# Performance work log

Measured on AMD Instinct MI355X. Metric: run time of the kernel, lower is better.

The kernel has to match this reference:

```python
import jax, jax.numpy as jnp
import numpy as np

B, N1, N2, D, H = 32, 512, 256, 256, 8
HD = D // H  # head dim = 32


def setup_inputs() -> dict:
    key = jax.random.key(0)
    ks = jax.random.split(key, 12)
    s = 0.05
    return {
        "x1": jax.random.normal(ks[0], (B, N1, D), jnp.float32),
        "x2": jax.random.normal(ks[1], (B, N2, D), jnp.float32),
        "r_w1": jax.random.normal(ks[2], (D, 2 * D), jnp.float32) * s,
        "r_b1": jnp.zeros((D,), jnp.float32),
        "ln_g": jnp.ones((D,), jnp.float32),
        "ln_b": jnp.zeros((D,), jnp.float32),
        "r_w2": jax.random.normal(ks[3], (4, D), jnp.float32) * s,
        "r_b2": jnp.zeros((4,), jnp.float32),
        "lf_w": jax.random.normal(ks[4], (D, D), jnp.float32) * s,
        "lf_b": jnp.zeros((D,), jnp.float32),
        "af2_w": jax.random.normal(ks[5], (D, D), jnp.float32) * s,
        "af2_b": jnp.zeros((D,), jnp.float32),
        "af3_w": jax.random.normal(ks[6], (N1, D), jnp.float32) * s,  # Linear(dim, num_pathway)
        "af3_b": jnp.zeros((N1,), jnp.float32),
        "attn_in_w": jax.random.normal(ks[7], (3 * D, D), jnp.float32) * s,
        "attn_in_b": jnp.zeros((3 * D,), jnp.float32),
        "attn_out_w": jax.random.normal(ks[8], (D, D), jnp.float32) * s,
        "attn_out_b": jnp.zeros((D,), jnp.float32),
    }


def _layernorm(x, g, b, eps=1e-5):
    mu = x.mean(-1, keepdims=True)
    var = ((x - mu) ** 2).mean(-1, keepdims=True)
    return (x - mu) * jax.lax.rsqrt(var + eps) * g + b


def reference(x1, x2, r_w1, r_b1, ln_g, ln_b, r_w2, r_b2,
              lf_w, lf_b, af2_w, af2_b, af3_w, af3_b,
              attn_in_w, attn_in_b, attn_out_w, attn_out_b):
    b, n1, d = x1.shape
    n2 = x2.shape[1]

    # ---- RoutingNetwork: mean-pool both modalities, small MLP, softmax ----
    m = jnp.concatenate([x1.mean(1), x2.mean(1)], axis=-1)        # [b, 2d]
    h = jax.nn.gelu(_layernorm(m @ r_w1.T + r_b1, ln_g, ln_b), approximate=False)
    logits = h @ r_w2.T + r_b2                                     # [b, 4]
    w = jax.nn.softmax(logits, axis=-1)                            # [b, 4]

    z = jnp.concatenate([x1, x2], axis=1)                          # [b, n1+n2, d]

    # ---- Expert 0: LinearFusion (dropout off at eval) ----
    lf = jax.nn.elu(z @ lf_w.T + lf_b)
    g0, i0 = lf[:, :n1, :], lf[:, n1:, :]

    # ---- Expert 1: AddFusion, n1 >= n2 branch (n2 == dim required) ----
    a1 = jax.nn.elu(x1 @ af2_w.T + af2_b)                          # [b, n1, d]
    a2 = jax.nn.elu(jnp.einsum('bnd,pn->bdp', x2, af3_w) + af3_b)  # [b, d, n1]
    a2 = a2.transpose(0, 2, 1)                                     # [b, n1, d]
    x_out = a1 + a2
    g1, i1 = x_out, x_out[:, :n2, :]

    # ---- Expert 2: AttentionFusion (MHA, 8 heads, self-attn over concat) ----
    qkv = z @ attn_in_w.T + attn_in_b                              # [b, S, 3d]
    q, k, v = jnp.split(qkv, 3, axis=-1)
    S = n1 + n2
    q = q.reshape(b, S, H, HD)
    k = k.reshape(b, S, H, HD)
    v = v.reshape(b, S, H, HD)
    scores = jnp.einsum('bqhd,bkhd->bhqk', q, k) / np.sqrt(HD)
    attn = jax.nn.softmax(scores, axis=-1)
    o = jnp.einsum('bhqk,bkhd->bqhd', attn, v).reshape(b, S, d)
    o = o @ attn_out_w.T + attn_out_b
    g2, i2 = o[:, :n1, :], o[:, n1:, :]

    # ---- Expert 3: IdentityFusion ----
    g3, i3 = x1, x2

    # ---- Soft-routing weighted combine ----
    gene_all = jnp.stack([g0, g1, g2, g3], axis=1)                 # [b, 4, n1, d]
    img_all = jnp.stack([i0, i1, i2, i3], axis=1)                  # [b, 4, n2, d]
    we = w[:, :, None, None]
    gene = (gene_all * we).sum(axis=1)
    img = (img_all * we).sum(axis=1)
    return gene, img
```

## Files before the change

kernel.cpp:

```cpp
#include <hip/hip_runtime.h>
#include <hip/hip_bf16.h>
#include <math.h>

#define B_ 32
#define N1_ 512
#define N2_ 256
#define D_ 256
#define S_ 768
#define IMG_OFF 4194304
#define SCALE_ 0.17677669529663689f

typedef __attribute__((ext_vector_type(8))) short bf16x8;
typedef __attribute__((ext_vector_type(4))) float f32x4;
#define MFMA16(a, b, c) __builtin_amdgcn_mfma_f32_16x16x32_bf16(a, b, c, 0, 0, 0)

__device__ __forceinline__ ushort f2b(float f) {
  __hip_bfloat16 h = __float2bfloat16(f);
  return __builtin_bit_cast(ushort, h);
}
__device__ __forceinline__ float eluf(float v) { return v > 0.f ? v : expm1f(v); }

__global__ __launch_bounds__(256) void k_cvt(const float* __restrict__ src,
                                             ushort* __restrict__ zb,
                                             int shift, int boff) {
  int j = blockIdx.x*256 + threadIdx.x;
  int b = j >> shift;
  int rj = j & ((1 << shift) - 1);
  const float4* s = (const float4*)src + (size_t)j*2;
  float4 v0 = s[0], v1 = s[1];
  uint4 pk;
  pk.x = (uint)f2b(v0.x) | ((uint)f2b(v0.y) << 16);
  pk.y = (uint)f2b(v0.z) | ((uint)f2b(v0.w) << 16);
  pk.z = (uint)f2b(v1.x) | ((uint)f2b(v1.y) << 16);
  pk.w = (uint)f2b(v1.z) | ((uint)f2b(v1.w) << 16);
  *(uint4*)(zb + (size_t)b*196608 + boff + (size_t)rj*8) = pk;
}

__global__ __launch_bounds__(256) void k_wcvt(const float* __restrict__ lf_w,
                                              const float* __restrict__ af2_w,
                                              const float* __restrict__ af3_w,
                                              const float* __restrict__ attn_in_w,
                                              const float* __restrict__ attn_out_w,
                                              ushort* __restrict__ wb) {
  int g = blockIdx.x*256 + threadIdx.x;
  int e0 = g*4;
  const float* src; int loc; float sc = 1.f;
  if (e0 < 65536)       { src = lf_w;       loc = e0; }
  else if (e0 < 131072) { src = af2_w;      loc = e0 - 65536; }
  else if (e0 < 262144) { src = af3_w;      loc = e0 - 131072; }
  else if (e0 < 458752) { src = attn_in_w;  loc = e0 - 262144; if (loc < 65536) sc = SCALE_; }
  else                  { src = attn_out_w; loc = e0 - 458752; }
  float4 v = *(const float4*)(src + loc);
  *(ushort4*)(wb + e0) = make_ushort4(f2b(v.x*sc), f2b(v.y*sc), f2b(v.z*sc), f2b(v.w*sc));
}

__global__ __launch_bounds__(256) void k_mean(const float* __restrict__ x1,
                                              const float* __restrict__ x2,
                                              float* __restrict__ mp) {
  int b = blockIdx.x >> 3;
  int s = blockIdx.x & 7;
  int d = threadIdx.x;
  float s1 = 0.f;
  const float* p1 = x1 + ((size_t)(b*N1_ + s*64))*D_ + d;
  for (int n = 0; n < 64; ++n) s1 += p1[(size_t)n*D_];
  float s2 = 0.f;
  const float* p2 = x2 + ((size_t)(b*N2_ + s*32))*D_ + d;
  for (int n = 0; n < 32; ++n) s2 += p2[(size_t)n*D_];
  mp[(size_t)(b*8+s)*512 + d]       = s1 * (1.0f/512.0f);
  mp[(size_t)(b*8+s)*512 + 256 + d] = s2 * (1.0f/256.0f);
}

__global__ __launch_bounds__(256) void k_head(const float* __restrict__ mp, const float* __restrict__ r_w1,
                       const float* __restrict__ r_b1, const float* __restrict__ ln_g,
                       const float* __restrict__ ln_b, const float* __restrict__ r_w2,
                       const float* __restrict__ r_b2, float* __restrict__ wout) {
  int b = blockIdx.x;
  int j = threadIdx.x;
  __shared__ float ms[512];
  __shared__ float red[256];
  float a0 = 0.f, a1 = 0.f;
  for (int s = 0; s < 8; ++s) {
    a0 += mp[(size_t)(b*8+s)*512 + j];
    a1 += mp[(size_t)(b*8+s)*512 + 256 + j];
  }
  ms[j] = a0; ms[j+256] = a1;
  __syncthreads();
  float acc = r_b1[j];
  const float* wrow = r_w1 + (size_t)j*512;
  for (int k = 0; k < 512; ++k) acc += ms[k]*wrow[k];
  red[j] = acc; __syncthreads();
  for (int off=128; off>0; off>>=1){ if (j<off) red[j]+=red[j+off]; __syncthreads(); }
  float mu = red[0] * (1.f/256.f); __syncthreads();
  float cd = acc - mu;
  red[j] = cd*cd; __syncthreads();
  for (int off=128; off>0; off>>=1){ if (j<off) red[j]+=red[j+off]; __syncthreads(); }
  float var = red[0]*(1.f/256.f); __syncthreads();
  float xn = cd * rsqrtf(var + 1e-5f) * ln_g[j] + ln_b[j];
  float h = 0.5f*xn*(1.f+erff(xn*0.70710678118654752f));
  float lg[4];
  for (int e=0;e<4;++e){
    red[j] = h * r_w2[e*256 + j]; __syncthreads();
    for (int off=128; off>0; off>>=1){ if (j<off) red[j]+=red[j+off]; __syncthreads(); }
    lg[e] = red[0] + r_b2[e]; __syncthreads();
  }
  if (j==0){
    float mx = fmaxf(fmaxf(lg[0],lg[1]),fmaxf(lg[2],lg[3]));
    float e0=expf(lg[0]-mx),e1=expf(lg[1]-mx),e2=expf(lg[2]-mx),e3=expf(lg[3]-mx);
    float s=e0+e1+e2+e3;
    wout[b*4+0]=e0/s; wout[b*4+1]=e1/s; wout[b*4+2]=e2/s; wout[b*4+3]=e3/s;
  }
}

__global__ __launch_bounds__(256) void k_lf(const ushort* __restrict__ zb, const ushort* __restrict__ wb,
                     const float* __restrict__ x1, const float* __restrict__ x2,
                     const float* __restrict__ lf_b,
                     const float* __restrict__ wgt, float* __restrict__ out) {
  int dt = blockIdx.x, nt = blockIdx.y, b = blockIdx.z;
  int tid = threadIdx.x;
  int lane = tid & 63, wid = tid >> 6;
  int wm = wid >> 1, wn = wid & 1;
  int l15 = lane & 15, quad = lane >> 4;
  __shared__ __align__(16) ushort As[64][72];
  __shared__ __align__(16) ushort Ws[64][72];
  f32x4 acc[2][2] = {};
  int n0 = nt*64, d0 = dt*64;
  int sr = tid >> 2, scg = (tid & 3) * 16;
  const ushort* arow = zb + (size_t)b*196608 + (size_t)(n0+sr)*256;
  const ushort* wrow = wb + (size_t)(d0+sr)*256;
  for (int k0 = 0; k0 < 256; k0 += 64) {
    *(uint4*)&As[sr][scg]   = *(const uint4*)(arow + k0 + scg);
    *(uint4*)&As[sr][scg+8] = *(const uint4*)(arow + k0 + scg + 8);
    *(uint4*)&Ws[sr][scg]   = *(const uint4*)(wrow + k0 + scg);
    *(uint4*)&Ws[sr][scg+8] = *(const uint4*)(wrow + k0 + scg + 8);
    __syncthreads();
    #pragma unroll
    for (int kc = 0; kc < 2; ++kc) {
      bf16x8 a0f = *(bf16x8*)&As[wm*32 + l15][kc*32 + quad*8];
      bf16x8 a1f = *(bf16x8*)&As[wm*32 + 16 + l15][kc*32 + quad*8];
      bf16x8 b0f = *(bf16x8*)&Ws[wn*32 + l15][kc*32 + quad*8];
      bf16x8 b1f = *(bf16x8*)&Ws[wn*32 + 16 + l15][kc*32 + quad*8];
      acc[0][0] = MFMA16(a0f, b0f, acc[0][0]);
      acc[0][1] = MFMA16(a0f, b1f, acc[0][1]);
      acc[1][0] = MFMA16(a1f, b0f, acc[1][0]);
      acc[1][1] = MFMA16(a1f, b1f, acc[1][1]);
    }
    __syncthreads();
  }
  float w0 = wgt[b*4+0], w3 = wgt[b*4+3];
  #pragma unroll
  for (int im = 0; im < 2; ++im) {
    #pragma unroll
    for (int reg = 0; reg < 4; ++reg) {
      int n = n0 + wm*32 + im*16 + quad*4 + reg;
      const float* zr = (n<N1_)? x1 + ((size_t)(b*N1_+n))*D_ : x2 + ((size_t)(b*N2_+(n-N1_)))*D_;
      float* orw = (n<N1_)? out + ((size_t)(b*N1_+n))*D_
                          : out + (size_t)IMG_OFF + ((size_t)(b*N2_+(n-N1_)))*D_;
      #pragma unroll
      for (int in = 0; in < 2; ++in) {
        int d = d0 + wn*32 + in*16 + l15;
        float v = acc[im][in][reg] + lf_b[d];
        orw[d] = w0*eluf(v) + w3*zr[d];
      }
    }
  }
}

__global__ __launch_bounds__(256) void k_xout(const ushort* __restrict__ zb, const ushort* __restrict__ wb,
                       const float* __restrict__ af2_b, const float* __restrict__ af3_b,
                       const float* __restrict__ wgt, float* __restrict__ out) {
  int dt = blockIdx.x, nt = blockIdx.y, b = blockIdx.z;
  int tid = threadIdx.x;
  int lane = tid & 63, wid = tid >> 6;
  int wm = wid >> 1, wn = wid & 1;
  int l15 = lane & 15, quad = lane >> 4;
  __shared__ __align__(16) ushort As1[64][72];
  __shared__ __align__(16) ushort Ws1[64][72];
  __shared__ __align__(16) ushort As2[64][72];
  __shared__ __align__(16) ushort Ws2[64][72];
  f32x4 acc1[2][2] = {}, acc2[2][2] = {};
  int n0 = nt*64, d0 = dt*64;
  int sr = tid >> 2, scg = (tid & 3) * 16;
  const ushort* a1row = zb + (size_t)b*196608 + (size_t)(n0+sr)*256;
  const ushort* w1row = wb + 65536 + (size_t)(d0+sr)*256;
  const ushort* a2row = wb + 131072 + (size_t)(n0+sr)*256;
  for (int k0 = 0; k0 < 256; k0 += 64) {
    *(uint4*)&As1[sr][scg]   = *(const uint4*)(a1row + k0 + scg);
    *(uint4*)&As1[sr][scg+8] = *(const uint4*)(a1row + k0 + scg + 8);
    *(uint4*)&Ws1[sr][scg]   = *(const uint4*)(w1row + k0 + scg);
    *(uint4*)&Ws1[sr][scg+8] = *(const uint4*)(w1row + k0 + scg + 8);
    *(uint4*)&As2[sr][scg]   = *(const uint4*)(a2row + k0 + scg);
    *(uint4*)&As2[sr][scg+8] = *(const uint4*)(a2row + k0 + scg + 8);
    {
      const ushort* x2r = zb + (size_t)b*196608 + 131072 + (size_t)(k0+sr)*256 + d0 + scg;
      uint4 va = *(const uint4*)x2r;
      uint4 vb = *(const uint4*)(x2r + 8);
      const ushort* ea = (const ushort*)&va;
      const ushort* eb = (const ushort*)&vb;
      #pragma unroll
      for (int i = 0; i < 8; ++i) Ws2[scg + i][sr] = ea[i];
      #pragma unroll
      for (int i = 0; i < 8; ++i) Ws2[scg + 8 + i][sr] = eb[i];
    }
    __syncthreads();
    #pragma unroll
    for (int kc = 0; kc < 2; ++kc) {
      bf16x8 a10 = *(bf16x8*)&As1[wm*32 + l15][kc*32 + quad*8];
      bf16x8 a11 = *(bf16x8*)&As1[wm*32 + 16 + l15][kc*32 + quad*8];
      bf16x8 b10 = *(bf16x8*)&Ws1[wn*32 + l15][kc*32 + quad*8];
      bf16x8 b11 = *(bf16x8*)&Ws1[wn*32 + 16 + l15][kc*32 + quad*8];
      acc1[0][0] = MFMA16(a10, b10, acc1[0][0]);
      acc1[0][1] = MFMA16(a10, b11, acc1[0][1]);
      acc1[1][0] = MFMA16(a11, b10, acc1[1][0]);
      acc1[1][1] = MFMA16(a11, b11, acc1[1][1]);
      bf16x8 a20 = *(bf16x8*)&As2[wm*32 + l15][kc*32 + quad*8];
      bf16x8 a21 = *(bf16x8*)&As2[wm*32 + 16 + l15][kc*32 + quad*8];
      bf16x8 b20 = *(bf16x8*)&Ws2[wn*32 + l15][kc*32 + quad*8];
      bf16x8 b21 = *(bf16x8*)&Ws2[wn*32 + 16 + l15][kc*32 + quad*8];
      acc2[0][0] = MFMA16(a20, b20, acc2[0][0]);
      acc2[0][1] = MFMA16(a20, b21, acc2[0][1]);
      acc2[1][0] = MFMA16(a21, b20, acc2[1][0]);
      acc2[1][1] = MFMA16(a21, b21, acc2[1][1]);
    }
    __syncthreads();
  }
  float w1v = wgt[b*4+1];
  #pragma unroll
  for (int im = 0; im < 2; ++im) {
    #pragma unroll
    for (int reg = 0; reg < 4; ++reg) {
      int n = n0 + wm*32 + im*16 + quad*4 + reg;
      float* grow = out + ((size_t)(b*N1_+n))*D_;
      float* irow = (n<N2_)? (out + (size_t)IMG_OFF + ((size_t)(b*N2_+n))*D_) : nullptr;
      float b3 = af3_b[n];
      #pragma unroll
      for (int in = 0; in < 2; ++in) {
        int d = d0 + wn*32 + in*16 + l15;
        float xo = eluf(acc1[im][in][reg] + af2_b[d]) + eluf(acc2[im][in][reg] + b3);
        grow[d] += w1v*xo;
        if (irow) irow[d] += w1v*xo;
      }
    }
  }
}

__global__ __launch_bounds__(256) void k_qkv(const ushort* __restrict__ zb, const ushort* __restrict__ wb,
                      const float* __restrict__ bias,
                      ushort* __restrict__ qws, ushort* __restrict__ kws,
                      ushort* __restrict__ vtws) {
  int ct = blockIdx.x, nt = blockIdx.y, b = blockIdx.z;
  int tid = threadIdx.x;
  int lane = tid & 63, wid = tid >> 6;
  int wm = wid >> 1, wn = wid & 1;
  int l15 = lane & 15, quad = lane >> 4;
  __shared__ __align__(16) ushort As[64][72];
  __shared__ __align__(16) ushort Ws[64][72];
  f32x4 acc[2][2] = {};
  int n0 = nt*64, c0b = ct*64;
  int sr = tid >> 2, scg = (tid & 3) * 16;
  const ushort* arow = zb + (size_t)b*196608 + (size_t)(n0+sr)*256;
  const ushort* wrow = wb + 262144 + (size_t)(c0b+sr)*256;
  for (int k0 = 0; k0 < 256; k0 += 64) {
    *(uint4*)&As[sr][scg]   = *(const uint4*)(arow + k0 + scg);
    *(uint4*)&As[sr][scg+8] = *(const uint4*)(arow + k0 + scg + 8);
    *(uint4*)&Ws[sr][scg]   = *(const uint4*)(wrow + k0 + scg);
    *(uint4*)&Ws[sr][scg+8] = *(const uint4*)(wrow + k0 + scg + 8);
    __syncthreads();
    #pragma unroll
    for (int kc = 0; kc < 2; ++kc) {
      bf16x8 a0f = *(bf16x8*)&As[wm*32 + l15][kc*32 + quad*8];
      bf16x8 a1f = *(bf16x8*)&As[wm*32 + 16 + l15][kc*32 + quad*8];
      bf16x8 b0f = *(bf16x8*)&Ws[wn*32 + l15][kc*32 + quad*8];
      bf16x8 b1f = *(bf16x8*)&Ws[wn*32 + 16 + l15][kc*32 + quad*8];
      acc[0][0] = MFMA16(a0f, b0f, acc[0][0]);
      acc[0][1] = MFMA16(a0f, b1f, acc[0][1]);
      acc[1][0] = MFMA16(a1f, b0f, acc[1][0]);
      acc[1][1] = MFMA16(a1f, b1f, acc[1][1]);
    }
    __syncthreads();
  }
  if (ct < 8) {
    ushort* dst = (ct < 4) ? qws : kws;
    int coff = (ct < 4) ? 0 : 256;
    float bsc = (ct < 4) ? SCALE_ : 1.f;
    #pragma unroll
    for (int im = 0; im < 2; ++im) {
      #pragma unroll
      for (int reg = 0; reg < 4; ++reg) {
        int n = n0 + wm*32 + im*16 + quad*4 + reg;
        #pragma unroll
        for (int in = 0; in < 2; ++in) {
          int c = c0b + wn*32 + in*16 + l15;
          dst[((size_t)(b*S_)+n)*256 + (c - coff)] = f2b(acc[im][in][reg] + bias[c]*bsc);
        }
      }
    }
  } else {
    #pragma unroll
    for (int im = 0; im < 2; ++im) {
      int nb = n0 + wm*32 + im*16 + quad*4;
      #pragma unroll
      for (int in = 0; in < 2; ++in) {
        int c = c0b + wn*32 + in*16 + l15;
        float bs = bias[c];
        int vcol = c - 512;
        int h = vcol >> 5, d = vcol & 31;
        uint2 pk;
        pk.x = (uint)f2b(acc[im][in][0] + bs) | ((uint)f2b(acc[im][in][1] + bs) << 16);
        pk.y = (uint)f2b(acc[im][in][2] + bs) | ((uint)f2b(acc[im][in][3] + bs) << 16);
        *(uint2*)&vtws[(((size_t)(b*8+h))*32 + d)*S_ + nb] = pk;
      }
    }
  }
}

__global__ __launch_bounds__(256) void k_attn(const ushort* __restrict__ qws,
                                              const ushort* __restrict__ kws,
                                              const ushort* __restrict__ vtws,
                                              ushort* __restrict__ obuf) {
  int qt = blockIdx.x, h = blockIdx.y, b = blockIdx.z;
  int tid = threadIdx.x;
  int lane = tid & 63, w = tid >> 6;
  int l15 = lane & 15, quad = lane >> 4;
  __shared__ __align__(16) ushort Ks[64][40];
  __shared__ __align__(16) ushort Vts[32][72];
  __shared__ __align__(16) ushort Ps[4][16][72];

  bf16x8 bq[2];
  #pragma unroll
  for (int u = 0; u < 2; ++u) {
    int qn = qt*128 + w*32 + u*16 + l15;
    bq[u] = *(const bf16x8*)(qws + ((size_t)(b*S_)+qn)*256 + h*32 + quad*8);
  }
  f32x4 ao[2][2] = {};
  float m_run[2] = {-INFINITY, -INFINITY};
  float l_run[2] = {0.f, 0.f};

  int skr = tid >> 2, skc = (tid & 3) * 8;
  int svd = tid >> 3, svn = (tid & 7) * 8;

  for (int kt = 0; kt < 12; ++kt) {
    __syncthreads();
    *(uint4*)&Ks[skr][skc] =
        *(const uint4*)(kws + ((size_t)(b*S_) + kt*64 + skr)*256 + h*32 + skc);
    *(uint4*)&Vts[svd][svn] =
        *(const uint4*)(vtws + (((size_t)(b*8+h))*32 + svd)*S_ + kt*64 + svn);
    __syncthreads();

    bf16x8 ak[4];
    #pragma unroll
    for (int t = 0; t < 4; ++t) ak[t] = *(bf16x8*)&Ks[t*16 + l15][quad*8];
    bf16x8 av[2][2];
    #pragma unroll
    for (int im = 0; im < 2; ++im)
      #pragma unroll
      for (int kc = 0; kc < 2; ++kc)
        av[im][kc] = *(bf16x8*)&Vts[im*16 + l15][kc*32 + quad*8];

    #pragma unroll
    for (int u = 0; u < 2; ++u) {
      f32x4 sf[4];
      #pragma unroll
      for (int t = 0; t < 4; ++t) {
        f32x4 z = {0.f, 0.f, 0.f, 0.f};
        sf[t] = MFMA16(ak[t], bq[u], z);
      }
      float m0 = sf[0][0];
      #pragma unroll
      for (int t = 0; t < 4; ++t)
        #pragma unroll
        for (int r = 0; r < 4; ++r) m0 = fmaxf(m0, sf[t][r]);
      m0 = fmaxf(m0, __shfl_xor(m0, 16, 64));
      m0 = fmaxf(m0, __shfl_xor(m0, 32, 64));
      float mnew = fmaxf(m_run[u], m0);
      float al = __expf(m_run[u] - mnew);
      m_run[u] = mnew;
      float ls = 0.f;
      ushort pu[4][4];
      #pragma unroll
      for (int t = 0; t < 4; ++t)
        #pragma unroll
        for (int r = 0; r < 4; ++r) {
          float p = __expf(sf[t][r] - mnew);
          ls += p;
          pu[t][r] = f2b(p);
        }
      ls += __shfl_xor(ls, 16, 64);
      ls += __shfl_xor(ls, 32, 64);
      l_run[u] = l_run[u]*al + ls;
      #pragma unroll
      for (int t = 0; t < 4; ++t) {
        uint2 pk;
        pk.x = (uint)pu[t][0] | ((uint)pu[t][1] << 16);
        pk.y = (uint)pu[t][2] | ((uint)pu[t][3] << 16);
        *(uint2*)&Ps[w][l15][t*16 + quad*4] = pk;
      }
      #pragma unroll
      for (int e = 0; e < 4; ++e) { ao[u][0][e] *= al; ao[u][1][e] *= al; }
      #pragma unroll
      for (int kc = 0; kc < 2; ++kc) {
        bf16x8 bp = *(bf16x8*)&Ps[w][l15][kc*32 + quad*8];
        ao[u][0] = MFMA16(av[0][kc], bp, ao[u][0]);
        ao[u][1] = MFMA16(av[1][kc], bp, ao[u][1]);
      }
    }
  }
  #pragma unroll
  for (int u = 0; u < 2; ++u) {
    float linv = 1.f / l_run[u];
    int n = qt*128 + w*32 + u*16 + l15;
    ushort* orow = obuf + ((size_t)(b*S_)+n)*256 + h*32;
    #pragma unroll
    for (int im = 0; im < 2; ++im) {
      uint2 pk;
      pk.x = (uint)f2b(ao[u][im][0]*linv) | ((uint)f2b(ao[u][im][1]*linv) << 16);
      pk.y = (uint)f2b(ao[u][im][2]*linv) | ((uint)f2b(ao[u][im][3]*linv) << 16);
      *(uint2*)(orow + im*16 + quad*4) = pk;
    }
  }
}

__global__ __launch_bounds__(256) void k_proj(const ushort* __restrict__ obuf, const ushort* __restrict__ wb,
                       const float* __restrict__ bias, const float* __restrict__ wgt,
                       float* __restrict__ out) {
  int dt = blockIdx.x, nt = blockIdx.y, b = blockIdx.z;
  int tid = threadIdx.x;
  int lane = tid & 63, wid = tid >> 6;
  int wm = wid >> 1, wn = wid & 1;
  int l15 = lane & 15, quad = lane >> 4;
  __shared__ __align__(16) ushort As[64][72];
  __shared__ __align__(16) ushort Ws[64][72];
  f32x4 acc[2][2] = {};
  int n0 = nt*64, d0 = dt*64;
  int sr = tid >> 2, scg = (tid & 3) * 16;
  const ushort* arow = obuf + ((size_t)(b*S_) + n0 + sr)*256;
  const ushort* wrow = wb + 458752 + (size_t)(d0+sr)*256;
  for (int k0 = 0; k0 < 256; k0 += 64) {
    *(uint4*)&As[sr][scg]   = *(const uint4*)(arow + k0 + scg);
    *(uint4*)&As[sr][scg+8] = *(const uint4*)(arow + k0 + scg + 8);
    *(uint4*)&Ws[sr][scg]   = *(const uint4*)(wrow + k0 + scg);
    *(uint4*)&Ws[sr][scg+8] = *(const uint4*)(wrow + k0 + scg + 8);
    __syncthreads();
    #pragma unroll
    for (int kc = 0; kc < 2; ++kc) {
      bf16x8 a0f = *(bf16x8*)&As[wm*32 + l15][kc*32 + quad*8];
      bf16x8 a1f = *(bf16x8*)&As[wm*32 + 16 + l15][kc*32 + quad*8];
      bf16x8 b0f = *(bf16x8*)&Ws[wn*32 + l15][kc*32 + quad*8];
      bf16x8 b1f = *(bf16x8*)&Ws[wn*32 + 16 + l15][kc*32 + quad*8];
      acc[0][0] = MFMA16(a0f, b0f, acc[0][0]);
      acc[0][1] = MFMA16(a0f, b1f, acc[0][1]);
      acc[1][0] = MFMA16(a1f, b0f, acc[1][0]);
      acc[1][1] = MFMA16(a1f, b1f, acc[1][1]);
    }
    __syncthreads();
  }
  float w2v = wgt[b*4+2];
  #pragma unroll
  for (int im = 0; im < 2; ++im) {
    #pragma unroll
    for (int reg = 0; reg < 4; ++reg) {
      int n = n0 + wm*32 + im*16 + quad*4 + reg;
      float* orw = (n<N1_)? out + ((size_t)(b*N1_+n))*D_
                          : out + (size_t)IMG_OFF + ((size_t)(b*N2_+(n-N1_)))*D_;
      #pragma unroll
      for (int in = 0; in < 2; ++in) {
        int d = d0 + wn*32 + in*16 + l15;
        orw[d] += w2v*(acc[im][in][reg] + bias[d]);
      }
    }
  }
}

extern "C" void kernel_launch(void* const* d_in, const int* in_sizes, int n_in,
                              void* d_out, int out_size, void* d_ws, size_t ws_size,
                              hipStream_t stream) {
  const float* x1        = (const float*)d_in[0];
  const float* x2        = (const float*)d_in[1];
  const float* r_w1      = (const float*)d_in[2];
  const float* r_b1      = (const float*)d_in[3];
  const float* ln_g      = (const float*)d_in[4];
  const float* ln_b      = (const float*)d_in[5];
  const float* r_w2      = (const float*)d_in[6];
  const float* r_b2      = (const float*)d_in[7];
  const float* lf_w      = (const float*)d_in[8];
  const float* lf_b      = (const float*)d_in[9];
  const float* af2_w     = (const float*)d_in[10];
  const float* af2_b     = (const float*)d_in[11];
  const float* af3_w     = (const float*)d_in[12];
  const float* af3_b     = (const float*)d_in[13];
  const float* attn_in_w = (const float*)d_in[14];
  const float* attn_in_b = (const float*)d_in[15];
  const float* attn_out_w= (const float*)d_in[16];
  const float* attn_out_b= (const float*)d_in[17];
  float* out = (float*)d_out;

  float* ws_mp = (float*)d_ws;
  float* ws_w  = ws_mp + 131072;
  ushort* ws_qo = (ushort*)(ws_w + 128);
  ushort* ws_k  = ws_qo + (size_t)B_*S_*256;
  ushort* ws_vt = ws_k  + (size_t)B_*S_*256;
  ushort* ws_zb = ws_vt + (size_t)B_*S_*256;
  ushort* ws_wb = ws_zb + (size_t)B_*S_*256;

  k_cvt <<<dim3(2048), 256, 0, stream>>>(x1, ws_zb, 14, 0);
  k_cvt <<<dim3(1024), 256, 0, stream>>>(x2, ws_zb, 13, 131072);
  k_wcvt<<<dim3(512),  256, 0, stream>>>(lf_w, af2_w, af3_w, attn_in_w, attn_out_w, ws_wb);
  k_mean<<<dim3(B_*8), 256, 0, stream>>>(x1, x2, ws_mp);
  k_head<<<dim3(B_),   256, 0, stream>>>(ws_mp, r_w1, r_b1, ln_g, ln_b, r_w2, r_b2, ws_w);
  k_lf  <<<dim3(4,12,B_), 256, 0, stream>>>(ws_zb, ws_wb, x1, x2, lf_b, ws_w, out);
  k_xout<<<dim3(4,8,B_),  256, 0, stream>>>(ws_zb, ws_wb, af2_b, af3_b, ws_w, out);
  k_qkv <<<dim3(12,12,B_),256, 0, stream>>>(ws_zb, ws_wb, attn_in_b, ws_qo, ws_k, ws_vt);
  k_attn<<<dim3(6,8,B_),  256, 0, stream>>>(ws_qo, ws_k, ws_vt, ws_qo);
  k_proj<<<dim3(4,12,B_), 256, 0, stream>>>(ws_qo, attn_out_w ? ws_wb : ws_wb, attn_out_b, ws_w, out);
}
```

Before: 285.7 us.

## Fuse expert GEMMs into one output kernel and drop online softmax max

```diff
diff --git a/kernel.cpp b/kernel.cpp
--- a/kernel.cpp
+++ b/kernel.cpp
@@ -9,6 +9,7 @@
 #define S_ 768
 #define IMG_OFF 4194304
 #define SCALE_ 0.17677669529663689f
+#define QSCALE_ (0.17677669529663689f * 1.4426950408889634f)
 
 typedef __attribute__((ext_vector_type(8))) short bf16x8;
 typedef __attribute__((ext_vector_type(4))) float f32x4;
@@ -20,20 +21,48 @@
 }
 __device__ __forceinline__ float eluf(float v) { return v > 0.f ? v : expm1f(v); }
 
-__global__ __launch_bounds__(256) void k_cvt(const float* __restrict__ src,
-                                             ushort* __restrict__ zb,
-                                             int shift, int boff) {
-  int j = blockIdx.x*256 + threadIdx.x;
-  int b = j >> shift;
-  int rj = j & ((1 << shift) - 1);
-  const float4* s = (const float4*)src + (size_t)j*2;
-  float4 v0 = s[0], v1 = s[1];
-  uint4 pk;
-  pk.x = (uint)f2b(v0.x) | ((uint)f2b(v0.y) << 16);
-  pk.y = (uint)f2b(v0.z) | ((uint)f2b(v0.w) << 16);
-  pk.z = (uint)f2b(v1.x) | ((uint)f2b(v1.y) << 16);
-  pk.w = (uint)f2b(v1.z) | ((uint)f2b(v1.w) << 16);
-  *(uint4*)(zb + (size_t)b*196608 + boff + (size_t)rj*8) = pk;
+__global__ __launch_bounds__(256) void k_prep(const float* __restrict__ x1,
+                                              const float* __restrict__ x2,
+                                              ushort* __restrict__ zb,
+                                              float* __restrict__ mp) {
+  int b = blockIdx.x >> 3, s = blockIdx.x & 7;
+  int t = threadIdx.x;
+  int c = t & 63;
+  int rg = t >> 6;
+  __shared__ float red[4][260];
+  float4 s1 = {0.f, 0.f, 0.f, 0.f};
+  for (int i = 0; i < 16; ++i) {
+    int r = s*64 + rg*16 + i;
+    float4 v = *(const float4*)(x1 + ((size_t)(b*N1_) + r)*D_ + c*4);
+    s1.x += v.x; s1.y += v.y; s1.z += v.z; s1.w += v.w;
+    uint2 pk;
+    pk.x = (uint)f2b(v.x) | ((uint)f2b(v.y) << 16);
+    pk.y = (uint)f2b(v.z) | ((uint)f2b(v.w) << 16);
+    *(uint2*)(zb + (size_t)b*196608 + (size_t)r*256 + c*4) = pk;
+  }
+  red[rg][c*4+0] = s1.x; red[rg][c*4+1] = s1.y; red[rg][c*4+2] = s1.z; red[rg][c*4+3] = s1.w;
+  __syncthreads();
+  {
+    float v = red[0][t] + red[1][t] + red[2][t] + red[3][t];
+    mp[(size_t)(b*8+s)*512 + t] = v * (1.0f/512.0f);
+  }
+  __syncthreads();
+  float4 s2 = {0.f, 0.f, 0.f, 0.f};
+  for (int i = 0; i < 8; ++i) {
+    int r = s*32 + rg*8 + i;
+    float4 v = *(const float4*)(x2 + ((size_t)(b*N2_) + r)*D_ + c*4);
+    s2.x += v.x; s2.y += v.y; s2.z += v.z; s2.w += v.w;
+    uint2 pk;
+    pk.x = (uint)f2b(v.x) | ((uint)f2b(v.y) << 16);
+    pk.y = (uint)f2b(v.z) | ((uint)f2b(v.w) << 16);
+    *(uint2*)(zb + (size_t)b*196608 + (size_t)(512 + r)*256 + c*4) = pk;
+  }
+  red[rg][c*4+0] = s2.x; red[rg][c*4+1] = s2.y; red[rg][c*4+2] = s2.z; red[rg][c*4+3] = s2.w;
+  __syncthreads();
+  {
+    float v = red[0][t] + red[1][t] + red[2][t] + red[3][t];
+    mp[(size_t)(b*8+s)*512 + 256 + t] = v * (1.0f/256.0f);
+  }
 }
 
 __global__ __launch_bounds__(256) void k_wcvt(const float* __restrict__ lf_w,
@@ -48,26 +77,10 @@
   if (e0 < 65536)       { src = lf_w;       loc = e0; }
   else if (e0 < 131072) { src = af2_w;      loc = e0 - 65536; }
   else if (e0 < 262144) { src = af3_w;      loc = e0 - 131072; }
-  else if (e0 < 458752) { src = attn_in_w;  loc = e0 - 262144; if (loc < 65536) sc = SCALE_; }
+  else if (e0 < 458752) { src = attn_in_w;  loc = e0 - 262144; if (loc < 65536) sc = QSCALE_; }
   else                  { src = attn_out_w; loc = e0 - 458752; }
   float4 v = *(const float4*)(src + loc);
   *(ushort4*)(wb + e0) = make_ushort4(f2b(v.x*sc), f2b(v.y*sc), f2b(v.z*sc), f2b(v.w*sc));
-}
-
-__global__ __launch_bounds__(256) void k_mean(const float* __restrict__ x1,
-                                              const float* __restrict__ x2,
-                                              float* __restrict__ mp) {
-  int b = blockIdx.x >> 3;
-  int s = blockIdx.x & 7;
-  int d = threadIdx.x;
-  float s1 = 0.f;
-  const float* p1 = x1 + ((size_t)(b*N1_ + s*64))*D_ + d;
-  for (int n = 0; n < 64; ++n) s1 += p1[(size_t)n*D_];
-  float s2 = 0.f;
-  const float* p2 = x2 + ((size_t)(b*N2_ + s*32))*D_ + d;
-  for (int n = 0; n < 32; ++n) s2 += p2[(size_t)n*D_];
-  mp[(size_t)(b*8+s)*512 + d]       = s1 * (1.0f/512.0f);
-  mp[(size_t)(b*8+s)*512 + 256 + d] = s2 * (1.0f/256.0f);
 }
 
 __global__ __launch_bounds__(256) void k_head(const float* __restrict__ mp, const float* __restrict__ r_w1,
@@ -111,10 +124,181 @@
   }
 }
 
-__global__ __launch_bounds__(256) void k_lf(const ushort* __restrict__ zb, const ushort* __restrict__ wb,
-                     const float* __restrict__ x1, const float* __restrict__ x2,
-                     const float* __restrict__ lf_b,
-                     const float* __restrict__ wgt, float* __restrict__ out) {
+__global__ __launch_bounds__(256) void k_qkv(const ushort* __restrict__ zb, const ushort* __restrict__ wb,
+                      const float* __restrict__ bias,
+                      ushort* __restrict__ qo, ushort* __restrict__ kh,
+                      ushort* __restrict__ vt) {
+  int ct = blockIdx.x, nt = blockIdx.y, b = blockIdx.z;
+  int tid = threadIdx.x;
+  int lane = tid & 63, wid = tid >> 6;
+  int wm = wid >> 1, wn = wid & 1;
+  int l15 = lane & 15, quad = lane >> 4;
+  __shared__ __align__(16) ushort As[128][72];
+  __shared__ __align__(16) ushort Ws[128][72];
+  f32x4 acc[4][4] = {};
+  int n0 = nt*128, c0 = ct*128;
+  int sr = tid >> 1, sc = (tid & 1) * 32;
+  const ushort* arow = zb + (size_t)b*196608 + (size_t)(n0+sr)*256;
+  const ushort* wrow = wb + 262144 + (size_t)(c0+sr)*256;
+  for (int k0 = 0; k0 < 256; k0 += 64) {
+    #pragma unroll
+    for (int i = 0; i < 4; ++i) {
+      *(uint4*)&As[sr][sc + 8*i] = *(const uint4*)(arow + k0 + sc + 8*i);
+      *(uint4*)&Ws[sr][sc + 8*i] = *(const uint4*)(wrow + k0 + sc + 8*i);
+    }
+    __syncthreads();
+    #pragma unroll
+    for (int kc = 0; kc < 2; ++kc) {
+      bf16x8 af[4], bfr[4];
+      #pragma unroll
+      for (int im = 0; im < 4; ++im) af[im] = *(bf16x8*)&As[wm*64 + im*16 + l15][kc*32 + quad*8];
+      #pragma unroll
+      for (int in = 0; in < 4; ++in) bfr[in] = *(bf16x8*)&Ws[wn*64 + in*16 + l15][kc*32 + quad*8];
+      #pragma unroll
+      for (int im = 0; im < 4; ++im)
+        #pragma unroll
+        for (int in = 0; in < 4; ++in)
+          acc[im][in] = MFMA16(af[im], bfr[in], acc[im][in]);
+    }
+    __syncthreads();
+  }
+  if (ct < 2) {
+    #pragma unroll
+    for (int im = 0; im < 4; ++im)
+      #pragma unroll
+      for (int reg = 0; reg < 4; ++reg) {
+        int n = n0 + wm*64 + im*16 + quad*4 + reg;
+        #pragma unroll
+        for (int in = 0; in < 4; ++in) {
+          int c = c0 + wn*64 + in*16 + l15;
+          qo[((size_t)(b*S_)+n)*256 + c] = f2b(acc[im][in][reg] + bias[c]*QSCALE_);
+        }
+      }
+  } else if (ct < 4) {
+    #pragma unroll
+    for (int im = 0; im < 4; ++im)
+      #pragma unroll
+      for (int reg = 0; reg < 4; ++reg) {
+        int n = n0 + wm*64 + im*16 + quad*4 + reg;
+        #pragma unroll
+        for (int in = 0; in < 4; ++in) {
+          int c = c0 + wn*64 + in*16 + l15;
+          int kc2 = c - 256; int h = kc2 >> 5, d = kc2 & 31;
+          kh[(((size_t)(b*8+h))*S_ + n)*32 + d] = f2b(acc[im][in][reg] + bias[c]);
+        }
+      }
+  } else {
+    #pragma unroll
+    for (int im = 0; im < 4; ++im) {
+      int nb = n0 + wm*64 + im*16 + quad*4;
+      #pragma unroll
+      for (int in = 0; in < 4; ++in) {
+        int c = c0 + wn*64 + in*16 + l15;
+        float bs = bias[c];
+        int vcol = c - 512; int h = vcol >> 5, d = vcol & 31;
+        uint2 pk;
+        pk.x = (uint)f2b(acc[im][in][0] + bs) | ((uint)f2b(acc[im][in][1] + bs) << 16);
+        pk.y = (uint)f2b(acc[im][in][2] + bs) | ((uint)f2b(acc[im][in][3] + bs) << 16);
+        *(uint2*)&vt[(((size_t)(b*8+h))*32 + d)*S_ + nb] = pk;
+      }
+    }
+  }
+}
+
+__global__ __launch_bounds__(256) void k_attn(const ushort* __restrict__ qo,
+                                              const ushort* __restrict__ kh,
+                                              const ushort* __restrict__ vt,
+                                              ushort* __restrict__ obuf) {
+  int qhf = blockIdx.x, h = blockIdx.y, b = blockIdx.z;
+  int tid = threadIdx.x;
+  int lane = tid & 63, w = tid >> 6;
+  int l15 = lane & 15, quad = lane >> 4;
+  __shared__ __align__(16) ushort Ks[64][40];
+  __shared__ __align__(16) ushort Vts[32][72];
+  __shared__ __align__(16) ushort Ps[4][16][72];
+
+  int qbase = qhf*384 + w*96;
+  bf16x8 bq[6];
+  #pragma unroll
+  for (int u = 0; u < 6; ++u)
+    bq[u] = *(const bf16x8*)(qo + ((size_t)(b*S_) + qbase + u*16 + l15)*256 + h*32 + quad*8);
+
+  f32x4 ao[6][2] = {};
+  float lacc[6] = {};
+
+  int skr = tid >> 2, skc = (tid & 3) * 8;
+  int svd = tid >> 3, svn = (tid & 7) * 8;
+  const ushort* khb = kh + ((size_t)(b*8+h))*S_*32;
+  const ushort* vtb = vt + ((size_t)(b*8+h))*32*S_;
+
+  for (int kt = 0; kt < 12; ++kt) {
+    __syncthreads();
+    *(uint4*)&Ks[skr][skc] = *(const uint4*)(khb + (size_t)(kt*64 + skr)*32 + skc);
+    *(uint4*)&Vts[svd][svn] = *(const uint4*)(vtb + (size_t)svd*S_ + kt*64 + svn);
+    __syncthreads();
+
+    bf16x8 ak[4];
+    #pragma unroll
+    for (int t = 0; t < 4; ++t) ak[t] = *(bf16x8*)&Ks[t*16 + l15][quad*8];
+    bf16x8 av[2][2];
+    #pragma unroll
+    for (int im = 0; im < 2; ++im)
+      #pragma unroll
+      for (int kc = 0; kc < 2; ++kc)
+        av[im][kc] = *(bf16x8*)&Vts[im*16 + l15][kc*32 + quad*8];
+
+    #pragma unroll
+    for (int u = 0; u < 6; ++u) {
+      f32x4 sf[4];
+      #pragma unroll
+      for (int t = 0; t < 4; ++t) {
+        f32x4 z = {0.f, 0.f, 0.f, 0.f};
+        sf[t] = MFMA16(ak[t], bq[u], z);
+      }
+      #pragma unroll
+      for (int t = 0; t < 4; ++t) {
+        float p0 = __builtin_amdgcn_exp2f(sf[t][0]);
+        float p1 = __builtin_amdgcn_exp2f(sf[t][1]);
+        float p2 = __builtin_amdgcn_exp2f(sf[t][2]);
+        float p3 = __builtin_amdgcn_exp2f(sf[t][3]);
+        lacc[u] += (p0 + p1) + (p2 + p3);
+        uint2 pk;
+        pk.x = (uint)f2b(p0) | ((uint)f2b(p1) << 16);
+        pk.y = (uint)f2b(p2) | ((uint)f2b(p3) << 16);
+        *(uint2*)&Ps[w][l15][t*16 + quad*4] = pk;
+      }
+      #pragma unroll
+      for (int kc = 0; kc < 2; ++kc) {
+        bf16x8 bp = *(bf16x8*)&Ps[w][l15][kc*32 + quad*8];
+        ao[u][0] = MFMA16(av[0][kc], bp, ao[u][0]);
+        ao[u][1] = MFMA16(av[1][kc], bp, ao[u][1]);
+      }
+    }
+  }
+  #pragma unroll
+  for (int u = 0; u < 6; ++u) {
+    float l = lacc[u];
+    l += __shfl_xor(l, 16, 64);
+    l += __shfl_xor(l, 32, 64);
+    float linv = 1.f / l;
+    int n = qbase + u*16 + l15;
+    ushort* orow = obuf + ((size_t)(b*S_)+n)*256 + h*32;
+    #pragma unroll
+    for (int im = 0; im < 2; ++im) {
+      uint2 pk;
+      pk.x = (uint)f2b(ao[u][im][0]*linv) | ((uint)f2b(ao[u][im][1]*linv) << 16);
+      pk.y = (uint)f2b(ao[u][im][2]*linv) | ((uint)f2b(ao[u][im][3]*linv) << 16);
+      *(uint2*)(orow + im*16 + quad*4) = pk;
+    }
+  }
+}
+
+__global__ __launch_bounds__(256) void k_out(const ushort* __restrict__ zb, const ushort* __restrict__ wb,
+                      const ushort* __restrict__ ob,
+                      const float* __restrict__ x1, const float* __restrict__ x2,
+                      const float* __restrict__ lf_b, const float* __restrict__ af2_b,
+                      const float* __restrict__ af3_b, const float* __restrict__ ao_b,
+                      const float* __restrict__ wgt, float* __restrict__ out) {
   int dt = blockIdx.x, nt = blockIdx.y, b = blockIdx.z;
   int tid = threadIdx.x;
   int lane = tid & 63, wid = tid >> 6;
@@ -122,349 +306,132 @@
   int l15 = lane & 15, quad = lane >> 4;
   __shared__ __align__(16) ushort As[64][72];
   __shared__ __align__(16) ushort Ws[64][72];
-  f32x4 acc[2][2] = {};
+  f32x4 a_lf[2][2] = {}, a_a1[2][2] = {}, a_a2[2][2] = {}, a_pj[2][2] = {};
   int n0 = nt*64, d0 = dt*64;
+  int xr0 = ((nt < 8) ? nt : (nt - 8)) * 64;
   int sr = tid >> 2, scg = (tid & 3) * 16;
-  const ushort* arow = zb + (size_t)b*196608 + (size_t)(n0+sr)*256;
-  const ushort* wrow = wb + (size_t)(d0+sr)*256;
-  for (int k0 = 0; k0 < 256; k0 += 64) {
-    *(uint4*)&As[sr][scg]   = *(const uint4*)(arow + k0 + scg);
-    *(uint4*)&As[sr][scg+8] = *(const uint4*)(arow + k0 + scg + 8);
-    *(uint4*)&Ws[sr][scg]   = *(const uint4*)(wrow + k0 + scg);
-    *(uint4*)&Ws[sr][scg+8] = *(const uint4*)(wrow + k0 + scg + 8);
-    __syncthreads();
-    #pragma unroll
-    for (int kc = 0; kc < 2; ++kc) {
-      bf16x8 a0f = *(bf16x8*)&As[wm*32 + l15][kc*32 + quad*8];
-      bf16x8 a1f = *(bf16x8*)&As[wm*32 + 16 + l15][kc*32 + quad*8];
-      bf16x8 b0f = *(bf16x8*)&Ws[wn*32 + l15][kc*32 + quad*8];
-      bf16x8 b1f = *(bf16x8*)&Ws[wn*32 + 16 + l15][kc*32 + quad*8];
-      acc[0][0] = MFMA16(a0f, b0f, acc[0][0]);
-      acc[0][1] = MFMA16(a0f, b1f, acc[0][1]);
-      acc[1][0] = MFMA16(a1f, b0f, acc[1][0]);
-      acc[1][1] = MFMA16(a1f, b1f, acc[1][1]);
-    }
-    __syncthreads();
-  }
-  float w0 = wgt[b*4+0], w3 = wgt[b*4+3];
+
+  {
+    const ushort* ar = zb + (size_t)b*196608 + (size_t)(n0+sr)*256;
+    const ushort* wr = wb + (size_t)(d0+sr)*256;
+    for (int k0 = 0; k0 < 256; k0 += 64) {
+      *(uint4*)&As[sr][scg]   = *(const uint4*)(ar + k0 + scg);
+      *(uint4*)&As[sr][scg+8] = *(const uint4*)(ar + k0 + scg + 8);
+      *(uint4*)&Ws[sr][scg]   = *(const uint4*)(wr + k0 + scg);
+      *(uint4*)&Ws[sr][scg+8] = *(const uint4*)(wr + k0 + scg + 8);
+      __syncthreads();
+      #pragma unroll
+      for (int kc = 0; kc < 2; ++kc) {
+        bf16x8 a0 = *(bf16x8*)&As[wm*32 + l15][kc*32 + quad*8];
+        bf16x8 a1 = *(bf16x8*)&As[wm*32 + 16 + l15][kc*32 + quad*8];
+        bf16x8 b0 = *(bf16x8*)&Ws[wn*32 + l15][kc*32 + quad*8];
+        bf16x8 b1 = *(bf16x8*)&Ws[wn*32 + 16 + l15][kc*32 + quad*8];
+        a_lf[0][0] = MFMA16(a0, b0, a_lf[0][0]);
+        a_lf[0][1] = MFMA16(a0, b1, a_lf[0][1]);
+        a_lf[1][0] = MFMA16(a1, b0, a_lf[1][0]);
+        a_lf[1][1] = MFMA16(a1, b1, a_lf[1][1]);
+      }
+      __syncthreads();
+    }
+  }
+  {
+    const ushort* ar = zb + (size_t)b*196608 + (size_t)(xr0+sr)*256;
+    const ushort* wr = wb + 65536 + (size_t)(d0+sr)*256;
+    for (int k0 = 0; k0 < 256; k0 += 64) {
+      *(uint4*)&As[sr][scg]   = *(const uint4*)(ar + k0 + scg);
+      *(uint4*)&As[sr][scg+8] = *(const uint4*)(ar + k0 + scg + 8);
+      *(uint4*)&Ws[sr][scg]   = *(const uint4*)(wr + k0 + scg);
+      *(uint4*)&Ws[sr][scg+8] = *(const uint4*)(wr + k0 + scg + 8);
+      __syncthreads();
+      #pragma unroll
+      for (int kc = 0; kc < 2; ++kc) {
+        bf16x8 a0 = *(bf16x8*)&As[wm*32 + l15][kc*32 + quad*8];
+        bf16x8 a1 = *(bf16x8*)&As[wm*32 + 16 + l15][kc*32 + quad*8];
+        bf16x8 b0 = *(bf16x8*)&Ws[wn*32 + l15][kc*32 + quad*8];
+        bf16x8 b1 = *(bf16x8*)&Ws[wn*32 + 16 + l15][kc*32 + quad*8];
+        a_a1[0][0] = MFMA16(a0, b0, a_a1[0][0]);
+        a_a1[0][1] = MFMA16(a0, b1, a_a1[0][1]);
+        a_a1[1][0] = MFMA16(a1, b0, a_a1[1][0]);
+        a_a1[1][1] = MFMA16(a1, b1, a_a1[1][1]);
+      }
+      __syncthreads();
+    }
+  }
+  {
+    const ushort* ar = wb + 131072 + (size_t)(xr0+sr)*256;
+    for (int k0 = 0; k0 < 256; k0 += 64) {
+      *(uint4*)&As[sr][scg]   = *(const uint4*)(ar + k0 + scg);
+      *(uint4*)&As[sr][scg+8] = *(const uint4*)(ar + k0 + scg + 8);
+      {
+        const ushort* x2r = zb + (size_t)b*196608 + (size_t)(512 + k0 + sr)*256 + d0 + scg;
+        uint4 va = *(const uint4*)x2r;
+        uint4 vb = *(const uint4*)(x2r + 8);
+        const ushort* ea = (const ushort*)&va;
+        const ushort* eb = (const ushort*)&vb;
+        #pragma unroll
+        for (int i = 0; i < 8; ++i) Ws[scg + i][sr] = ea[i];
+        #pragma unroll
+        for (int i = 0; i < 8; ++i) Ws[scg + 8 + i][sr] = eb[i];
+      }
+      __syncthreads();
+      #pragma unroll
+      for (int kc = 0; kc < 2; ++kc) {
+        bf16x8 a0 = *(bf16x8*)&As[wm*32 + l15][kc*32 + quad*8];
+        bf16x8 a1 = *(bf16x8*)&As[wm*32 + 16 + l15][kc*32 + quad*8];
+        bf16x8 b0 = *(bf16x8*)&Ws[wn*32 + l15][kc*32 + quad*8];
+        bf16x8 b1 = *(bf16x8*)&Ws[wn*32 + 16 + l15][kc*32 + quad*8];
+        a_a2[0][0] = MFMA16(a0, b0, a_a2[0][0]);
+        a_a2[0][1] = MFMA16(a0, b1, a_a2[0][1]);
+        a_a2[1][0] = MFMA16(a1, b0, a_a2[1][0]);
+        a_a2[1][1] = MFMA16(a1, b1, a_a2[1][1]);
+      }
+      __syncthreads();
+    }
+  }
+  {
+    const ushort* ar = ob + ((size_t)(b*S_) + n0 + sr)*256;
+    const ushort* wr = wb + 458752 + (size_t)(d0+sr)*256;
+    for (int k0 = 0; k0 < 256; k0 += 64) {
+      *(uint4*)&As[sr][scg]   = *(const uint4*)(ar + k0 + scg);
+      *(uint4*)&As[sr][scg+8] = *(const uint4*)(ar + k0 + scg + 8);
+      *(uint4*)&Ws[sr][scg]   = *(const uint4*)(wr + k0 + scg);
+      *(uint4*)&Ws[sr][scg+8] = *(const uint4*)(wr + k0 + scg + 8);
+      __syncthreads();
+      #pragma unroll
+      for (int kc = 0; kc < 2; ++kc) {
+        bf16x8 a0 = *(bf16x8*)&As[wm*32 + l15][kc*32 + quad*8];
+        bf16x8 a1 = *(bf16x8*)&As[wm*32 + 16 + l15][kc*32 + quad*8];
+        bf16x8 b0 = *(bf16x8*)&Ws[wn*32 + l15][kc*32 + quad*8];
+        bf16x8 b1 = *(bf16x8*)&Ws[wn*32 + 16 + l15][kc*32 + quad*8];
+        a_pj[0][0] = MFMA16(a0, b0, a_pj[0][0]);
+        a_pj[0][1] = MFMA16(a0, b1, a_pj[0][1]);
+        a_pj[1][0] = MFMA16(a1, b0, a_pj[1][0]);
+        a_pj[1][1] = MFMA16(a1, b1, a_pj[1][1]);
+      }
+      __syncthreads();
+    }
+  }
+  float w0 = wgt[b*4+0], w1v = wgt[b*4+1], w2v = wgt[b*4+2], w3 = wgt[b*4+3];
   #pragma unroll
   for (int im = 0; im < 2; ++im) {
     #pragma unroll
     for (int reg = 0; reg < 4; ++reg) {
-      int n = n0 + wm*32 + im*16 + quad*4 + reg;
-      const float* zr = (n<N1_)? x1 + ((size_t)(b*N1_+n))*D_ : x2 + ((size_t)(b*N2_+(n-N1_)))*D_;
-      float* orw = (n<N1_)? out + ((size_t)(b*N1_+n))*D_
-                          : out + (size_t)IMG_OFF + ((size_t)(b*N2_+(n-N1_)))*D_;
+      int rl = wm*32 + im*16 + quad*4 + reg;
+      int n = n0 + rl;
+      int rx = xr0 + rl;
+      const float* zr; float* orw;
+      if (nt < 8) { zr = x1 + ((size_t)(b*N1_) + n)*D_;      orw = out + ((size_t)(b*N1_) + n)*D_; }
+      else { int j2 = n - 512; zr = x2 + ((size_t)(b*N2_) + j2)*D_;
+             orw = out + (size_t)IMG_OFF + ((size_t)(b*N2_) + j2)*D_; }
+      float b3 = af3_b[rx];
       #pragma unroll
       for (int in = 0; in < 2; ++in) {
         int d = d0 + wn*32 + in*16 + l15;
-        float v = acc[im][in][reg] + lf_b[d];
-        orw[d] = w0*eluf(v) + w3*zr[d];
-      }
-    }
-  }
-}
-
-__global__ __launch_bounds__(256) void k_xout(const ushort* __restrict__ zb, const ushort* __restrict__ wb,
-                       const float* __restrict__ af2_b, const float* __restrict__ af3_b,
-                       const float* __restrict__ wgt, float* __restrict__ out) {
-  int dt = blockIdx.x, nt = blockIdx.y, b = blockIdx.z;
-  int tid = threadIdx.x;
-  int lane = tid & 63, wid = tid >> 6;
-  int wm = wid >> 1, wn = wid & 1;
-  int l15 = lane & 15, quad = lane >> 4;
-  __shared__ __align__(16) ushort As1[64][72];
-  __shared__ __align__(16) ushort Ws1[64][72];
-  __shared__ __align__(16) ushort As2[64][72];
-  __shared__ __align__(16) ushort Ws2[64][72];
-  f32x4 acc1[2][2] = {}, acc2[2][2] = {};
-  int n0 = nt*64, d0 = dt*64;
-  int sr = tid >> 2, scg = (tid & 3) * 16;
-  const ushort* a1row = zb + (size_t)b*196608 + (size_t)(n0+sr)*256;
-  const ushort* w1row = wb + 65536 + (size_t)(d0+sr)*256;
-  const ushort* a2row = wb + 131072 + (size_t)(n0+sr)*256;
-  for (int k0 = 0; k0 < 256; k0 += 64) {
-    *(uint4*)&As1[sr][scg]   = *(const uint4*)(a1row + k0 + scg);
-    *(uint4*)&As1[sr][scg+8] = *(const uint4*)(a1row + k0 + scg + 8);
-    *(uint4*)&Ws1[sr][scg]   = *(const uint4*)(w1row + k0 + scg);
-    *(uint4*)&Ws1[sr][scg+8] = *(const uint4*)(w1row + k0 + scg + 8);
-    *(uint4*)&As2[sr][scg]   = *(const uint4*)(a2row + k0 + scg);
-    *(uint4*)&As2[sr][scg+8] = *(const uint4*)(a2row + k0 + scg + 8);
-    {
-      const ushort* x2r = zb + (size_t)b*196608 + 131072 + (size_t)(k0+sr)*256 + d0 + scg;
-      uint4 va = *(const uint4*)x2r;
-      uint4 vb = *(const uint4*)(x2r + 8);
-      const ushort* ea = (const ushort*)&va;
-      const ushort* eb = (const ushort*)&vb;
-      #pragma unroll
-      for (int i = 0; i < 8; ++i) Ws2[scg + i][sr] = ea[i];
-      #pragma unroll
-      for (int i = 0; i < 8; ++i) Ws2[scg + 8 + i][sr] = eb[i];
-    }
-    __syncthreads();
-    #pragma unroll
-    for (int kc = 0; kc < 2; ++kc) {
-      bf16x8 a10 = *(bf16x8*)&As1[wm*32 + l15][kc*32 + quad*8];
-      bf16x8 a11 = *(bf16x8*)&As1[wm*32 + 16 + l15][kc*32 + quad*8];
-      bf16x8 b10 = *(bf16x8*)&Ws1[wn*32 + l15][kc*32 + quad*8];
-      bf16x8 b11 = *(bf16x8*)&Ws1[wn*32 + 16 + l15][kc*32 + quad*8];
-      acc1[0][0] = MFMA16(a10, b10, acc1[0][0]);
-      acc1[0][1] = MFMA16(a10, b11, acc1[0][1]);
-      acc1[1][0] = MFMA16(a11, b10, acc1[1][0]);
-      acc1[1][1] = MFMA16(a11, b11, acc1[1][1]);
-      bf16x8 a20 = *(bf16x8*)&As2[wm*32 + l15][kc*32 + quad*8];
-      bf16x8 a21 = *(bf16x8*)&As2[wm*32 + 16 + l15][kc*32 + quad*8];
-      bf16x8 b20 = *(bf16x8*)&Ws2[wn*32 + l15][kc*32 + quad*8];
-      bf16x8 b21 = *(bf16x8*)&Ws2[wn*32 + 16 + l15][kc*32 + quad*8];
-      acc2[0][0] = MFMA16(a20, b20, acc2[0][0]);
-      acc2[0][1] = MFMA16(a20, b21, acc2[0][1]);
-      acc2[1][0] = MFMA16(a21, b20, acc2[1][0]);
-      acc2[1][1] = MFMA16(a21, b21, acc2[1][1]);
-    }
-    __syncthreads();
-  }
-  float w1v = wgt[b*4+1];
-  #pragma unroll
-  for (int im = 0; im < 2; ++im) {
-    #pragma unroll
-    for (int reg = 0; reg < 4; ++reg) {
-      int n = n0 + wm*32 + im*16 + quad*4 + reg;
-      float* grow = out + ((size_t)(b*N1_+n))*D_;
-      float* irow = (n<N2_)? (out + (size_t)IMG_OFF + ((size_t)(b*N2_+n))*D_) : nullptr;
-      float b3 = af3_b[n];
-      #pragma unroll
-      for (int in = 0; in < 2; ++in) {
-        int d = d0 + wn*32 + in*16 + l15;
-        float xo = eluf(acc1[im][in][reg] + af2_b[d]) + eluf(acc2[im][in][reg] + b3);
-        grow[d] += w1v*xo;
-        if (irow) irow[d] += w1v*xo;
-      }
-    }
-  }
-}
-
-__global__ __launch_bounds__(256) void k_qkv(const ushort* __restrict__ zb, const ushort* __restrict__ wb,
-                      const float* __restrict__ bias,
-                      ushort* __restrict__ qws, ushort* __restrict__ kws,
-                      ushort* __restrict__ vtws) {
-  int ct = blockIdx.x, nt = blockIdx.y, b = blockIdx.z;
-  int tid = threadIdx.x;
-  int lane = tid & 63, wid = tid >> 6;
-  int wm = wid >> 1, wn = wid & 1;
-  int l15 = lane & 15, quad = lane >> 4;
-  __shared__ __align__(16) ushort As[64][72];
-  __shared__ __align__(16) ushort Ws[64][72];
-  f32x4 acc[2][2] = {};
-  int n0 = nt*64, c0b = ct*64;
-  int sr = tid >> 2, scg = (tid & 3) * 16;
-  const ushort* arow = zb + (size_t)b*196608 + (size_t)(n0+sr)*256;
-  const ushort* wrow = wb + 262144 + (size_t)(c0b+sr)*256;
-  for (int k0 = 0; k0 < 256; k0 += 64) {
-    *(uint4*)&As[sr][scg]   = *(const uint4*)(arow + k0 + scg);
-    *(uint4*)&As[sr][scg+8] = *(const uint4*)(arow + k0 + scg + 8);
-    *(uint4*)&Ws[sr][scg]   = *(const uint4*)(wrow + k0 + scg);
-    *(uint4*)&Ws[sr][scg+8] = *(const uint4*)(wrow + k0 + scg + 8);
-    __syncthreads();
-    #pragma unroll
-    for (int kc = 0; kc < 2; ++kc) {
-      bf16x8 a0f = *(bf16x8*)&As[wm*32 + l15][kc*32 + quad*8];
-      bf16x8 a1f = *(bf16x8*)&As[wm*32 + 16 + l15][kc*32 + quad*8];
-      bf16x8 b0f = *(bf16x8*)&Ws[wn*32 + l15][kc*32 + quad*8];
-      bf16x8 b1f = *(bf16x8*)&Ws[wn*32 + 16 + l15][kc*32 + quad*8];
-      acc[0][0] = MFMA16(a0f, b0f, acc[0][0]);
-      acc[0][1] = MFMA16(a0f, b1f, acc[0][1]);
-      acc[1][0] = MFMA16(a1f, b0f, acc[1][0]);
-      acc[1][1] = MFMA16(a1f, b1f, acc[1][1]);
-    }
-    __syncthreads();
-  }
-  if (ct < 8) {
-    ushort* dst = (ct < 4) ? qws : kws;
-    int coff = (ct < 4) ? 0 : 256;
-    float bsc = (ct < 4) ? SCALE_ : 1.f;
-    #pragma unroll
-    for (int im = 0; im < 2; ++im) {
-      #pragma unroll
-      for (int reg = 0; reg < 4; ++reg) {
-        int n = n0 + wm*32 + im*16 + quad*4 + reg;
-        #pragma unroll
-        for (int in = 0; in < 2; ++in) {
-          int c = c0b + wn*32 + in*16 + l15;
-          dst[((size_t)(b*S_)+n)*256 + (c - coff)] = f2b(acc[im][in][reg] + bias[c]*bsc);
-        }
-      }
-    }
-  } else {
-    #pragma unroll
-    for (int im = 0; im < 2; ++im) {
-      int nb = n0 + wm*32 + im*16 + quad*4;
-      #pragma unroll
-      for (int in = 0; in < 2; ++in) {
-        int c = c0b + wn*32 + in*16 + l15;
-        float bs = bias[c];
-        int vcol = c - 512;
-        int h = vcol >> 5, d = vcol & 31;
-        uint2 pk;
-        pk.x = (uint)f2b(acc[im][in][0] + bs) | ((uint)f2b(acc[im][in][1] + bs) << 16);
-        pk.y = (uint)f2b(acc[im][in][2] + bs) | ((uint)f2b(acc[im][in][3] + bs) << 16);
-        *(uint2*)&vtws[(((size_t)(b*8+h))*32 + d)*S_ + nb] = pk;
-      }
-    }
-  }
-}
-
-__global__ __launch_bounds__(256) void k_attn(const ushort* __restrict__ qws,
-                                              const ushort* __restrict__ kws,
-                                              const ushort* __restrict__ vtws,
-                                              ushort* __restrict__ obuf) {
-  int qt = blockIdx.x, h = blockIdx.y, b = blockIdx.z;
-  int tid = threadIdx.x;
-  int lane = tid & 63, w = tid >> 6;
-  int l15 = lane & 15, quad = lane >> 4;
-  __shared__ __align__(16) ushort Ks[64][40];
-  __shared__ __align__(16) ushort Vts[32][72];
-  __shared__ __align__(16) ushort Ps[4][16][72];
-
-  bf16x8 bq[2];
-  #pragma unroll
-  for (int u = 0; u < 2; ++u) {
-    int qn = qt*128 + w*32 + u*16 + l15;
-    bq[u] = *(const bf16x8*)(qws + ((size_t)(b*S_)+qn)*256 + h*32 + quad*8);
-  }
-  f32x4 ao[2][2] = {};
-  float m_run[2] = {-INFINITY, -INFINITY};
-  float l_run[2] = {0.f, 0.f};
-
-  int skr = tid >> 2, skc = (tid & 3) * 8;
-  int svd = tid >> 3, svn = (tid & 7) * 8;
-
-  for (int kt = 0; kt < 12; ++kt) {
-    __syncthreads();
-    *(uint4*)&Ks[skr][skc] =
-        *(const uint4*)(kws + ((size_t)(b*S_) + kt*64 + skr)*256 + h*32 + skc);
-    *(uint4*)&Vts[svd][svn] =
-        *(const uint4*)(vtws + (((size_t)(b*8+h))*32 + svd)*S_ + kt*64 + svn);
-    __syncthreads();
-
-    bf16x8 ak[4];
-    #pragma unroll
-    for (int t = 0; t < 4; ++t) ak[t] = *(bf16x8*)&Ks[t*16 + l15][quad*8];
-    bf16x8 av[2][2];
-    #pragma unroll
-    for (int im = 0; im < 2; ++im)
-      #pragma unroll
-      for (int kc = 0; kc < 2; ++kc)
-        av[im][kc] = *(bf16x8*)&Vts[im*16 + l15][kc*32 + quad*8];
-
-    #pragma unroll
-    for (int u = 0; u < 2; ++u) {
-      f32x4 sf[4];
-      #pragma unroll
-      for (int t = 0; t < 4; ++t) {
-        f32x4 z = {0.f, 0.f, 0.f, 0.f};
-        sf[t] = MFMA16(ak[t], bq[u], z);
-      }
-      float m0 = sf[0][0];
-      #pragma unroll
-      for (int t = 0; t < 4; ++t)
-        #pragma unroll
-        for (int r = 0; r < 4; ++r) m0 = fmaxf(m0, sf[t][r]);
-      m0 = fmaxf(m0, __shfl_xor(m0, 16, 64));
-      m0 = fmaxf(m0, __shfl_xor(m0, 32, 64));
-      float mnew = fmaxf(m_run[u], m0);
-      float al = __expf(m_run[u] - mnew);
-      m_run[u] = mnew;
-      float ls = 0.f;
-      ushort pu[4][4];
-      #pragma unroll
-      for (int t = 0; t < 4; ++t)
-        #pragma unroll
-        for (int r = 0; r < 4; ++r) {
-          float p = __expf(sf[t][r] - mnew);
-          ls += p;
-          pu[t][r] = f2b(p);
-        }
-      ls += __shfl_xor(ls, 16, 64);
-      ls += __shfl_xor(ls, 32, 64);
-      l_run[u] = l_run[u]*al + ls;
-      #pragma unroll
-      for (int t = 0; t < 4; ++t) {
-        uint2 pk;
-        pk.x = (uint)pu[t][0] | ((uint)pu[t][1] << 16);
-        pk.y = (uint)pu[t][2] | ((uint)pu[t][3] << 16);
-        *(uint2*)&Ps[w][l15][t*16 + quad*4] = pk;
-      }
-      #pragma unroll
-      for (int e = 0; e < 4; ++e) { ao[u][0][e] *= al; ao[u][1][e] *= al; }
-      #pragma unroll
-      for (int kc = 0; kc < 2; ++kc) {
-        bf16x8 bp = *(bf16x8*)&Ps[w][l15][kc*32 + quad*8];
-        ao[u][0] = MFMA16(av[0][kc], bp, ao[u][0]);
-        ao[u][1] = MFMA16(av[1][kc], bp, ao[u][1]);
-      }
-    }
-  }
-  #pragma unroll
-  for (int u = 0; u < 2; ++u) {
-    float linv = 1.f / l_run[u];
-    int n = qt*128 + w*32 + u*16 + l15;
-    ushort* orow = obuf + ((size_t)(b*S_)+n)*256 + h*32;
-    #pragma unroll
-    for (int im = 0; im < 2; ++im) {
-      uint2 pk;
-      pk.x = (uint)f2b(ao[u][im][0]*linv) | ((uint)f2b(ao[u][im][1]*linv) << 16);
-      pk.y = (uint)f2b(ao[u][im][2]*linv) | ((uint)f2b(ao[u][im][3]*linv) << 16);
-      *(uint2*)(orow + im*16 + quad*4) = pk;
-    }
-  }
-}
-
-__global__ __launch_bounds__(256) void k_proj(const ushort* __restrict__ obuf, const ushort* __restrict__ wb,
-                       const float* __restrict__ bias, const float* __restrict__ wgt,
-                       float* __restrict__ out) {
-  int dt = blockIdx.x, nt = blockIdx.y, b = blockIdx.z;
-  int tid = threadIdx.x;
-  int lane = tid & 63, wid = tid >> 6;
-  int wm = wid >> 1, wn = wid & 1;
-  int l15 = lane & 15, quad = lane >> 4;
-  __shared__ __align__(16) ushort As[64][72];
-  __shared__ __align__(16) ushort Ws[64][72];
-  f32x4 acc[2][2] = {};
-  int n0 = nt*64, d0 = dt*64;
-  int sr = tid >> 2, scg = (tid & 3) * 16;
-  const ushort* arow = obuf + ((size_t)(b*S_) + n0 + sr)*256;
-  const ushort* wrow = wb + 458752 + (size_t)(d0+sr)*256;
-  for (int k0 = 0; k0 < 256; k0 += 64) {
-    *(uint4*)&As[sr][scg]   = *(const uint4*)(arow + k0 + scg);
-    *(uint4*)&As[sr][scg+8] = *(const uint4*)(arow + k0 + scg + 8);
-    *(uint4*)&Ws[sr][scg]   = *(const uint4*)(wrow + k0 + scg);
-    *(uint4*)&Ws[sr][scg+8] = *(const uint4*)(wrow + k0 + scg + 8);
-    __syncthreads();
-    #pragma unroll
-    for (int kc = 0; kc < 2; ++kc) {
-      bf16x8 a0f = *(bf16x8*)&As[wm*32 + l15][kc*32 + quad*8];
-      bf16x8 a1f = *(bf16x8*)&As[wm*32 + 16 + l15][kc*32 + quad*8];
-      bf16x8 b0f = *(bf16x8*)&Ws[wn*32 + l15][kc*32 + quad*8];
-      bf16x8 b1f = *(bf16x8*)&Ws[wn*32 + 16 + l15][kc*32 + quad*8];
-      acc[0][0] = MFMA16(a0f, b0f, acc[0][0]);
-      acc[0][1] = MFMA16(a0f, b1f, acc[0][1]);
-      acc[1][0] = MFMA16(a1f, b0f, acc[1][0]);
-      acc[1][1] = MFMA16(a1f, b1f, acc[1][1]);
-    }
-    __syncthreads();
-  }
-  float w2v = wgt[b*4+2];
-  #pragma unroll
-  for (int im = 0; im < 2; ++im) {
-    #pragma unroll
-    for (int reg = 0; reg < 4; ++reg) {
-      int n = n0 + wm*32 + im*16 + quad*4 + reg;
-      float* orw = (n<N1_)? out + ((size_t)(b*N1_+n))*D_
-                          : out + (size_t)IMG_OFF + ((size_t)(b*N2_+(n-N1_)))*D_;
-      #pragma unroll
-      for (int in = 0; in < 2; ++in) {
-        int d = d0 + wn*32 + in*16 + l15;
-        orw[d] += w2v*(acc[im][in][reg] + bias[d]);
+        float v = w0*eluf(a_lf[im][in][reg] + lf_b[d])
+                + w1v*(eluf(a_a1[im][in][reg] + af2_b[d]) + eluf(a_a2[im][in][reg] + b3))
+                + w2v*(a_pj[im][in][reg] + ao_b[d])
+                + w3*zr[d];
+        orw[d] = v;
       }
     }
   }
@@ -481,34 +448,28 @@
   const float* ln_b      = (const float*)d_in[5];
   const float* r_w2      = (const float*)d_in[6];
   const float* r_b2      = (const float*)d_in[7];
-  const float* lf_w      = (const float*)d_in[8];
   const float* lf_b      = (const float*)d_in[9];
-  const float* af2_w     = (const float*)d_in[10];
   const float* af2_b     = (const float*)d_in[11];
-  const float* af3_w     = (const float*)d_in[12];
   const float* af3_b     = (const float*)d_in[13];
-  const float* attn_in_w = (const float*)d_in[14];
   const float* attn_in_b = (const float*)d_in[15];
-  const float* attn_out_w= (const float*)d_in[16];
   const float* attn_out_b= (const float*)d_in[17];
   float* out = (float*)d_out;
 
   float* ws_mp = (float*)d_ws;
   float* ws_w  = ws_mp + 131072;
-  ushort* ws_qo = (ushort*)(ws_w + 128);
-  ushort* ws_k  = ws_qo + (size_t)B_*S_*256;
-  ushort* ws_vt = ws_k  + (size_t)B_*S_*256;
-  ushort* ws_zb = ws_vt + (size_t)B_*S_*256;
-  ushort* ws_wb = ws_zb + (size_t)B_*S_*256;
-
-  k_cvt <<<dim3(2048), 256, 0, stream>>>(x1, ws_zb, 14, 0);
-  k_cvt <<<dim3(1024), 256, 0, stream>>>(x2, ws_zb, 13, 131072);
-  k_wcvt<<<dim3(512),  256, 0, stream>>>(lf_w, af2_w, af3_w, attn_in_w, attn_out_w, ws_wb);
-  k_mean<<<dim3(B_*8), 256, 0, stream>>>(x1, x2, ws_mp);
+  ushort* ws_zb = (ushort*)(ws_w + 128);
+  ushort* ws_qo = ws_zb + (size_t)B_*S_*256;
+  ushort* ws_kh = ws_qo + (size_t)B_*S_*256;
+  ushort* ws_vt = ws_kh + (size_t)B_*S_*256;
+  ushort* ws_wb = ws_vt + (size_t)B_*S_*256;
+
+  k_prep<<<dim3(B_*8), 256, 0, stream>>>(x1, x2, ws_zb, ws_mp);
+  k_wcvt<<<dim3(512),  256, 0, stream>>>((const float*)d_in[8], (const float*)d_in[10],
+                                         (const float*)d_in[12], (const float*)d_in[14],
+                                         (const float*)d_in[16], ws_wb);
   k_head<<<dim3(B_),   256, 0, stream>>>(ws_mp, r_w1, r_b1, ln_g, ln_b, r_w2, r_b2, ws_w);
-  k_lf  <<<dim3(4,12,B_), 256, 0, stream>>>(ws_zb, ws_wb, x1, x2, lf_b, ws_w, out);
-  k_xout<<<dim3(4,8,B_),  256, 0, stream>>>(ws_zb, ws_wb, af2_b, af3_b, ws_w, out);
-  k_qkv <<<dim3(12,12,B_),256, 0, stream>>>(ws_zb, ws_wb, attn_in_b, ws_qo, ws_k, ws_vt);
-  k_attn<<<dim3(6,8,B_),  256, 0, stream>>>(ws_qo, ws_k, ws_vt, ws_qo);
-  k_proj<<<dim3(4,12,B_), 256, 0, stream>>>(ws_qo, attn_out_w ? ws_wb : ws_wb, attn_out_b, ws_w, out);
-}
+  k_qkv <<<dim3(6,6,B_), 256, 0, stream>>>(ws_zb, ws_wb, attn_in_b, ws_qo, ws_kh, ws_vt);
+  k_attn<<<dim3(2,8,B_), 256, 0, stream>>>(ws_qo, ws_kh, ws_vt, ws_qo);
+  k_out <<<dim3(4,12,B_),256, 0, stream>>>(ws_zb, ws_wb, ws_qo, x1, x2,
+                                           lf_b, af2_b, af3_b, attn_out_b, ws_w, out);
+}
```

Result: faster. 265.6 us (-7.0%).
